# Kernel tuning notes

Measured on AMD Instinct MI355X. Metric: run time of the kernel, lower is better.

Reference implementation:

```python
import jax, jax.numpy as jnp
import numpy as np

M, B, D, N = 8, 200000, 32, 100000
TINY = np.finfo(np.float32).tiny


def _vol(box):
    # box: (..., 2, D) with box[...,0,:]=z (min corner), box[...,1,:]=Z (max corner)
    side = jnp.clip(box[..., 1, :] - box[..., 0, :], 0.0, None)
    return jnp.prod(side, axis=-1)


def _intersection(a, b):
    z = jnp.maximum(a[..., 0, :], b[..., 0, :])
    Z = jnp.minimum(a[..., 1, :], b[..., 1, :])
    return jnp.stack((z, Z), axis=-2)


def setup_inputs() -> dict:
    key = jax.random.key(0)
    k1, k2, k3, k4 = jax.random.split(key, 4)
    z = jax.random.uniform(k1, (M, B, 1, D), dtype=jnp.float32) * 0.1
    Z = 0.9 + jax.random.uniform(k2, (M, B, 1, D), dtype=jnp.float32) * 0.1
    box_param = jnp.concatenate([z, Z], axis=2)  # (M, B, 2, D)
    weights = jax.random.normal(k3, (M,), dtype=jnp.float32)
    ids = jax.random.randint(k4, (N, 4), 0, B, dtype=jnp.int64)
    return {"box_param": box_param, "weights": weights, "ids": ids}


def reference(box_param, weights, ids):
    boxes = jnp.clip(box_param, 0.0, 1.0)  # default universe -> clamp to [0,1]
    w = jax.nn.softmax(weights)            # (M,)
    # default universe box has volume prod(1-0) = 1
    uz = jnp.zeros((D,), boxes.dtype)
    uZ = jnp.ones((D,), boxes.dtype)
    universe_vol = _vol(jnp.stack((uz, uZ), axis=-2))  # scalar 1.0

    def wsum(vols):  # vols: (M, N) -> (N,)
        return jnp.einsum('m,mn->n', w, vols)

    i0, i1, i2 = ids[:, 0], ids[:, 1], ids[:, 2]
    A = boxes[:, i0]   # (M, N, 2, D)
    Bb = boxes[:, i1]
    C = boxes[:, i2]

    unary_probs = wsum(_vol(A) / universe_vol)

    AiB = _intersection(A, Bb)
    two_vol = wsum(_vol(AiB) / universe_vol) + TINY
    two_div = wsum(_vol(A) / universe_vol) + TINY
    two_cond = jnp.exp(jnp.log(two_vol) - jnp.log(two_div))

    three_vol = wsum(_vol(_intersection(AiB, C)) / universe_vol) + TINY
    three_div = wsum(_vol(AiB) / universe_vol) + TINY
    three_cond = jnp.exp(jnp.log(three_vol) - jnp.log(three_div))

    unary_mask = i0 == i1
    three_mask = i1 != i2
    two_mask = jnp.logical_and(~three_mask, ~unary_mask)
    # torch writes unary, then two, then three -> three takes precedence
    probs = jnp.where(three_mask, three_cond,
            jnp.where(two_mask, two_cond,
            jnp.where(unary_mask, unary_probs, 0.0)))
    return probs
```

## Files before the change

kernel.cpp:

```cpp
#include <hip/hip_runtime.h>
#include <hip/hip_bf16.h>


#define MM 8
#define BB 200000
#define DD 32

__global__ __launch_bounds__(256) void box_triples_kernel(
    const float* __restrict__ box,
    const float* __restrict__ wts,
    const int*   __restrict__ ids,
    float*       __restrict__ out,
    int N)
{
    const int lane = threadIdx.x & 63;
    const int wave = threadIdx.x >> 6;
    const int n = blockIdx.x * (blockDim.x >> 6) + wave;
    if (n >= N) return;

    float wraw[MM];
    #pragma unroll
    for (int m = 0; m < MM; ++m) wraw[m] = wts[m];
    float wmax = wraw[0];
    #pragma unroll
    for (int m = 1; m < MM; ++m) wmax = fmaxf(wmax, wraw[m]);
    float esum = 0.f;
    float e[MM];
    #pragma unroll
    for (int m = 0; m < MM; ++m) { e[m] = expf(wraw[m] - wmax); esum += e[m]; }
    const float einv = 1.0f / esum;

    const int4 idv = ((const int4*)ids)[n];
    const int i0 = idv.x, i1 = idv.y, i2 = idv.z;

    const int msub = lane >> 5;
    const int d    = lane & 31;

    float sA = 0.f, sAB = 0.f, sABC = 0.f;

    #pragma unroll
    for (int mb = 0; mb < MM; mb += 2) {
        const int m = mb + msub;
        const int rowA = (m * BB + i0) * (2 * DD) + d;
        const int rowB = (m * BB + i1) * (2 * DD) + d;
        const int rowC = (m * BB + i2) * (2 * DD) + d;

        float zA = box[rowA], ZA = box[rowA + DD];
        float zB = box[rowB], ZB = box[rowB + DD];
        float zC = box[rowC], ZC = box[rowC + DD];

        zA = fminf(fmaxf(zA, 0.f), 1.f);  ZA = fminf(fmaxf(ZA, 0.f), 1.f);
        zB = fminf(fmaxf(zB, 0.f), 1.f);  ZB = fminf(fmaxf(ZB, 0.f), 1.f);
        zC = fminf(fmaxf(zC, 0.f), 1.f);  ZC = fminf(fmaxf(ZC, 0.f), 1.f);

        const float zAB  = fmaxf(zA, zB);
        const float ZAB  = fminf(ZA, ZB);
        const float zABC = fmaxf(zAB, zC);
        const float ZABC = fminf(ZAB, ZC);

        float sdA   = fmaxf(ZA   - zA,   0.f);
        float sdAB  = fmaxf(ZAB  - zAB,  0.f);
        float sdABC = fmaxf(ZABC - zABC, 0.f);

        #pragma unroll
        for (int off = 1; off < 32; off <<= 1) {
            sdA   *= __shfl_xor(sdA,   off);
            sdAB  *= __shfl_xor(sdAB,  off);
            sdABC *= __shfl_xor(sdABC, off);
        }

        const float w_lo = e[mb]     * einv;
        const float w_hi = e[mb + 1] * einv;
        const float wm = msub ? w_hi : w_lo;

        sA   += wm * sdA;
        sAB  += wm * sdAB;
        sABC += wm * sdABC;
    }

    sA   += __shfl_xor(sA,   32);
    sAB  += __shfl_xor(sAB,  32);
    sABC += __shfl_xor(sABC, 32);

    const float TINY = 1.1754943508222875e-38f;
    float res;
    if (i1 != i2) {
        res = (sABC + TINY) / (sAB + TINY);
    } else if (i0 != i1) {
        res = (sAB + TINY) / (sA + TINY);
    } else {
        res = sA;
    }

    if (lane == 0) out[n] = res;
}

extern "C" void kernel_launch(void* const* d_in, const int* in_sizes, int n_in,
                              void* d_out, int out_size, void* d_ws, size_t ws_size,
                              hipStream_t stream) {
    const float* box = (const float*)d_in[0];
    const float* wts = (const float*)d_in[1];
    const int*   ids = (const int*)d_in[2];
    float* out = (float*)d_out;
    const int N = out_size;

    const int wavesPerBlock = 4;
    const int blocks = (N + wavesPerBlock - 1) / wavesPerBlock;
    box_triples_kernel<<<blocks, 256, 0, stream>>>(box, wts, ids, out, N);
}
```

Before: 531.8 us.

## Map 8 lanes per model with float4 loads and distributed softmax

Reassigns lanes so each wave covers all 8 models at once: 8 lanes per model, each loading four dimensions of every box with float4 vector loads, instead of looping over the models two at a time with scalar loads. The per-lane products then need only a 3-step shuffle reduction plus a 3-step cross-model sum, replacing the 4 iterations of 5-step shuffle products. The softmax is computed across lanes with shuffles and __expf rather than by every lane for all 8 weights. All loads can now be issued up front, which gives more memory-level parallelism, at the cost of slightly different exp precision.

```diff
diff --git a/kernel.cpp b/kernel.cpp
--- a/kernel.cpp
+++ b/kernel.cpp
@@ -18,69 +18,63 @@
     const int n = blockIdx.x * (blockDim.x >> 6) + wave;
     if (n >= N) return;
 
-    float wraw[MM];
-    #pragma unroll
-    for (int m = 0; m < MM; ++m) wraw[m] = wts[m];
-    float wmax = wraw[0];
-    #pragma unroll
-    for (int m = 1; m < MM; ++m) wmax = fmaxf(wmax, wraw[m]);
-    float esum = 0.f;
-    float e[MM];
-    #pragma unroll
-    for (int m = 0; m < MM; ++m) { e[m] = expf(wraw[m] - wmax); esum += e[m]; }
-    const float einv = 1.0f / esum;
+    const int m = lane >> 3;
+    const int t = lane & 7;
 
     const int4 idv = ((const int4*)ids)[n];
     const int i0 = idv.x, i1 = idv.y, i2 = idv.z;
 
-    const int msub = lane >> 5;
-    const int d    = lane & 31;
+    const int baseA = (m * BB + i0) * (2 * DD) + t * 4;
+    const int baseB = (m * BB + i1) * (2 * DD) + t * 4;
+    const int baseC = (m * BB + i2) * (2 * DD) + t * 4;
 
-    float sA = 0.f, sAB = 0.f, sABC = 0.f;
+    const float4 zA4 = *(const float4*)(box + baseA);
+    const float4 ZA4 = *(const float4*)(box + baseA + DD);
+    const float4 zB4 = *(const float4*)(box + baseB);
+    const float4 ZB4 = *(const float4*)(box + baseB + DD);
+    const float4 zC4 = *(const float4*)(box + baseC);
+    const float4 ZC4 = *(const float4*)(box + baseC + DD);
+
+    float wl = wts[m];
+    float wmax = wl;
+    #pragma unroll
+    for (int off = 8; off < 64; off <<= 1) wmax = fmaxf(wmax, __shfl_xor(wmax, off));
+    float ew = __expf(wl - wmax);
+    float esum = ew;
+    #pragma unroll
+    for (int off = 8; off < 64; off <<= 1) esum += __shfl_xor(esum, off);
+    const float w = ew / esum;
+
+    float pA = 1.f, pAB = 1.f, pABC = 1.f;
+    #define CL(x) fminf(fmaxf((x), 0.f), 1.f)
+    #define COMP(c) { \
+        const float za = CL(zA4.c), Za = CL(ZA4.c); \
+        const float zb = CL(zB4.c), Zb = CL(ZB4.c); \
+        const float zc = CL(zC4.c), Zc = CL(ZC4.c); \
+        const float zab  = fmaxf(za, zb),  Zab  = fminf(Za, Zb); \
+        const float zabc = fmaxf(zab, zc), Zabc = fminf(Zab, Zc); \
+        pA   *= fmaxf(Za   - za,   0.f); \
+        pAB  *= fmaxf(Zab  - zab,  0.f); \
+        pABC *= fmaxf(Zabc - zabc, 0.f); \
+    }
+    COMP(x) COMP(y) COMP(z) COMP(w)
+    #undef COMP
+    #undef CL
 
     #pragma unroll
-    for (int mb = 0; mb < MM; mb += 2) {
-        const int m = mb + msub;
-        const int rowA = (m * BB + i0) * (2 * DD) + d;
-        const int rowB = (m * BB + i1) * (2 * DD) + d;
-        const int rowC = (m * BB + i2) * (2 * DD) + d;
-
-        float zA = box[rowA], ZA = box[rowA + DD];
-        float zB = box[rowB], ZB = box[rowB + DD];
-        float zC = box[rowC], ZC = box[rowC + DD];
-
-        zA = fminf(fmaxf(zA, 0.f), 1.f);  ZA = fminf(fmaxf(ZA, 0.f), 1.f);
-        zB = fminf(fmaxf(zB, 0.f), 1.f);  ZB = fminf(fmaxf(ZB, 0.f), 1.f);
-        zC = fminf(fmaxf(zC, 0.f), 1.f);  ZC = fminf(fmaxf(ZC, 0.f), 1.f);
-
-        const float zAB  = fmaxf(zA, zB);
-        const float ZAB  = fminf(ZA, ZB);
-        const float zABC = fmaxf(zAB, zC);
-        const float ZABC = fminf(ZAB, ZC);
-
-        float sdA   = fmaxf(ZA   - zA,   0.f);
-        float sdAB  = fmaxf(ZAB  - zAB,  0.f);
-        float sdABC = fmaxf(ZABC - zABC, 0.f);
-
-        #pragma unroll
-        for (int off = 1; off < 32; off <<= 1) {
-            sdA   *= __shfl_xor(sdA,   off);
-            sdAB  *= __shfl_xor(sdAB,  off);
-            sdABC *= __shfl_xor(sdABC, off);
-        }
-
-        const float w_lo = e[mb]     * einv;
-        const float w_hi = e[mb + 1] * einv;
-        const float wm = msub ? w_hi : w_lo;
-
-        sA   += wm * sdA;
-        sAB  += wm * sdAB;
-        sABC += wm * sdABC;
+    for (int off = 1; off < 8; off <<= 1) {
+        pA   *= __shfl_xor(pA,   off);
+        pAB  *= __shfl_xor(pAB,  off);
+        pABC *= __shfl_xor(pABC, off);
     }
 
-    sA   += __shfl_xor(sA,   32);
-    sAB  += __shfl_xor(sAB,  32);
-    sABC += __shfl_xor(sABC, 32);
+    float sA = w * pA, sAB = w * pAB, sABC = w * pABC;
+    #pragma unroll
+    for (int off = 8; off < 64; off <<= 1) {
+        sA   += __shfl_xor(sA,   off);
+        sAB  += __shfl_xor(sAB,  off);
+        sABC += __shfl_xor(sABC, off);
+    }
 
     const float TINY = 1.1754943508222875e-38f;
     float res;
```

Result: no change. 528.4 us (-0.6%).
